# Optimization experiments

Hardware: AMD Instinct MI355X
Metric: run time of the kernel (lower is better)

Reference implementation:

```python
import jax, jax.numpy as jnp
import numpy as np

N_NODES = 50000
N_EDGES = 800000
D = 128
N_LAYERS = 3
EPS = 1e-5


def _layer_norm(x, g, b):
    mu = jnp.mean(x, axis=-1, keepdims=True)
    var = jnp.mean(jnp.square(x - mu), axis=-1, keepdims=True)
    return (x - mu) * jax.lax.rsqrt(var + EPS) * g + b


def _sage_layer(h, src, dst, wl, bl_, wr, g, b):
    # mean aggregation of neighbor (source) features at destination nodes
    msg = h[src]                                             # [E, D] irregular gather
    agg = jax.ops.segment_sum(msg, dst, num_segments=N_NODES)
    deg = jax.ops.segment_sum(jnp.ones((src.shape[0],), h.dtype), dst, num_segments=N_NODES)
    mean = agg / jnp.maximum(deg, 1.0)[:, None]
    # SAGEConv: lin_l(mean_neigh) + lin_r(x); lin_r has no bias
    out = mean @ wl.T + bl_ + h @ wr.T
    h_new = jax.nn.relu(_layer_norm(out, g, b))
    return h + h_new                                          # residual (dims match)


def setup_inputs() -> dict:
    key = jax.random.key(0)
    ks = jax.random.split(key, 5)
    scale = 1.0 / np.sqrt(D)
    node_features = jax.random.normal(ks[0], (N_NODES, D), dtype=jnp.float32)
    edge_index = jax.random.randint(ks[1], (2, N_EDGES), 0, N_NODES, dtype=jnp.int64)
    Wl = jax.random.normal(ks[2], (N_LAYERS, D, D), dtype=jnp.float32) * scale
    Wr = jax.random.normal(ks[3], (N_LAYERS, D, D), dtype=jnp.float32) * scale
    bl = jnp.zeros((N_LAYERS, D), dtype=jnp.float32)
    gamma = jnp.ones((N_LAYERS, D), dtype=jnp.float32)
    beta = jnp.zeros((N_LAYERS, D), dtype=jnp.float32)
    return {"node_features": node_features, "edge_index": edge_index,
            "Wl": Wl, "bl": bl, "Wr": Wr, "gamma": gamma, "beta": beta}


def reference(node_features, edge_index, Wl, bl, Wr, gamma, beta):
    src, dst = edge_index[0], edge_index[1]
    h = node_features
    for i in range(N_LAYERS):
        h = _sage_layer(h, src, dst, Wl[i], bl[i], Wr[i], gamma[i], beta[i])
    return h
```

## Files before the change

### kernel.cpp

```cpp
#include <hip/hip_runtime.h>

#define N_NODES 50000
#define N_EDGES 800000
#define D       128
#define THREADS 256
#define EPS     1e-5f
#define SCAN_B  196
#define MTILES  3125

typedef __attribute__((ext_vector_type(8))) __bf16  bf16x8;
typedef __attribute__((ext_vector_type(8))) short   short8;
typedef __attribute__((ext_vector_type(4))) float   f32x4;
typedef __attribute__((ext_vector_type(4))) unsigned int u32x4;

__device__ inline unsigned int bfround(float x) {
    unsigned int u = __float_as_uint(x);
    return (u + 0x7FFFu + ((u >> 16) & 1u)) >> 16;
}
__device__ inline unsigned int packbf(float x) {
    unsigned int hi = bfround(x);
    float lo = x - __uint_as_float(hi << 16);
    return (hi << 16) | (bfround(lo) & 0xFFFFu);
}
__device__ inline float unpackbf(unsigned int u) {
    return __uint_as_float(u & 0xFFFF0000u) + __uint_as_float(u << 16);
}


__global__ void count_kernel(const int* __restrict__ dst, int* __restrict__ deg) {
    int e = blockIdx.x * 256 + threadIdx.x;
    if (e < N_EDGES) atomicAdd(&deg[dst[e]], 1);
}

__global__ void block_reduce_kernel(const int* __restrict__ deg, int* __restrict__ bsum) {
    __shared__ int red[256];
    int i = blockIdx.x * 256 + threadIdx.x;
    red[threadIdx.x] = (i < N_NODES) ? deg[i] : 0;
    __syncthreads();
    for (int off = 128; off > 0; off >>= 1) {
        if (threadIdx.x < off) red[threadIdx.x] += red[threadIdx.x + off];
        __syncthreads();
    }
    if (threadIdx.x == 0) bsum[blockIdx.x] = red[0];
}

__global__ void block_scan_kernel(const int* __restrict__ bsum, int* __restrict__ bbase) {
    __shared__ int s[256];
    const int t = threadIdx.x;
    const int v = (t < SCAN_B) ? bsum[t] : 0;
    s[t] = v;
    __syncthreads();
    for (int off = 1; off < 256; off <<= 1) {
        int add = (t >= off) ? s[t - off] : 0;
        __syncthreads();
        s[t] += add;
        __syncthreads();
    }
    if (t < SCAN_B) bbase[t] = s[t] - v;
}

__global__ void expand_kernel(const int* __restrict__ deg, const int* __restrict__ bbase,
                              int* __restrict__ row_start, int* __restrict__ cursor) {
    __shared__ int s[256];
    const int t = threadIdx.x;
    const int i = blockIdx.x * 256 + t;
    const int v = (i < N_NODES) ? deg[i] : 0;
    s[t] = v;
    __syncthreads();
    for (int off = 1; off < 256; off <<= 1) {
        int add = (t >= off) ? s[t - off] : 0;
        __syncthreads();
        s[t] += add;
        __syncthreads();
    }
    const int excl = bbase[blockIdx.x] + s[t] - v;
    if (i < N_NODES) { row_start[i] = excl; cursor[i] = excl; }
    if (i == N_NODES - 1) row_start[N_NODES] = excl + v;
}

__global__ void fill_kernel(const int* __restrict__ src, const int* __restrict__ dst,
                            int* __restrict__ cursor, int* __restrict__ ssrc) {
    int e = blockIdx.x * 256 + threadIdx.x;
    if (e < N_EDGES) {
        int d = dst[e];
        int p = atomicAdd(&cursor[d], 1);
        __builtin_nontemporal_store(src[e], &ssrc[p]);
    }
}


__global__ void wprep_kernel(const float* __restrict__ Wl, const float* __restrict__ Wr,
                             unsigned short* __restrict__ Whi, unsigned short* __restrict__ Wlo) {
    int t = blockIdx.x * 256 + threadIdx.x;
    if (t >= 3 * 128 * 256) return;
    const int L = t >> 15;
    const int r = t & 32767;
    const int j = r >> 8;
    const int k = r & 255;
    const float x = (k < 128) ? Wl[((size_t)L * 128 + j) * 128 + k]
                              : Wr[((size_t)L * 128 + j) * 128 + (k - 128)];
    const unsigned int p = packbf(x);
    Whi[t] = (unsigned short)(p >> 16);
    Wlo[t] = (unsigned short)(p & 0xFFFFu);
}

__global__ void cvt0_kernel(const float* __restrict__ nf,
                            unsigned int* __restrict__ Apk,
                            unsigned short* __restrict__ Hh) {
    int t = blockIdx.x * 256 + threadIdx.x;
    if (t >= N_NODES * 32) return;
    const int n  = t >> 5;
    const int k4 = (t & 31) * 4;
    const float4 v = *reinterpret_cast<const float4*>(nf + (size_t)n * D + k4);
    u32x4 o;
    o.x = packbf(v.x); o.y = packbf(v.y); o.z = packbf(v.z); o.w = packbf(v.w);
    *reinterpret_cast<u32x4*>(Apk + (size_t)n * 128 + k4) = o;
    uint2 hh;
    hh.x = (o.x >> 16) | (o.y & 0xFFFF0000u);
    hh.y = (o.z >> 16) | (o.w & 0xFFFF0000u);
    *reinterpret_cast<uint2*>((unsigned int*)Hh + (size_t)n * 64 + (k4 >> 1)) = hh;
}


__global__ __launch_bounds__(256, 8)
void agg_kernel(const unsigned short* __restrict__ Hh,
                unsigned short* __restrict__ Mb,
                const int* __restrict__ row_start, const int* __restrict__ ssrc) {
    const int lane = threadIdx.x & 63;
    const int wave = threadIdx.x >> 6;
    const int n = blockIdx.x * 4 + wave;
    if (n >= N_NODES) return;
    const int e0 = __builtin_amdgcn_readfirstlane(row_start[n]);
    const int e1 = __builtin_amdgcn_readfirstlane(row_start[n + 1]);
    const unsigned int* __restrict__ H = (const unsigned int*)Hh + lane;

    float a0 = 0.f, a1 = 0.f;
    #pragma unroll 1
    for (int e = e0; e < e1; e += 16) {
        const int el = e1 - 1;
        const int s0  = ssrc[min(e + 0,  el)];
        const int s1  = ssrc[min(e + 1,  el)];
        const int s2  = ssrc[min(e + 2,  el)];
        const int s3  = ssrc[min(e + 3,  el)];
        const int s4  = ssrc[min(e + 4,  el)];
        const int s5  = ssrc[min(e + 5,  el)];
        const int s6  = ssrc[min(e + 6,  el)];
        const int s7  = ssrc[min(e + 7,  el)];
        const int s8  = ssrc[min(e + 8,  el)];
        const int s9  = ssrc[min(e + 9,  el)];
        const int s10 = ssrc[min(e + 10, el)];
        const int s11 = ssrc[min(e + 11, el)];
        const int s12 = ssrc[min(e + 12, el)];
        const int s13 = ssrc[min(e + 13, el)];
        const int s14 = ssrc[min(e + 14, el)];
        const int s15 = ssrc[min(e + 15, el)];
        const unsigned int v0  = H[(size_t)s0  * 64];
        const unsigned int v1  = H[(size_t)s1  * 64];
        const unsigned int v2  = H[(size_t)s2  * 64];
        const unsigned int v3  = H[(size_t)s3  * 64];
        const unsigned int v4  = H[(size_t)s4  * 64];
        const unsigned int v5  = H[(size_t)s5  * 64];
        const unsigned int v6  = H[(size_t)s6  * 64];
        const unsigned int v7  = H[(size_t)s7  * 64];
        const unsigned int v8  = H[(size_t)s8  * 64];
        const unsigned int v9  = H[(size_t)s9  * 64];
        const unsigned int v10 = H[(size_t)s10 * 64];
        const unsigned int v11 = H[(size_t)s11 * 64];
        const unsigned int v12 = H[(size_t)s12 * 64];
        const unsigned int v13 = H[(size_t)s13 * 64];
        const unsigned int v14 = H[(size_t)s14 * 64];
        const unsigned int v15 = H[(size_t)s15 * 64];
        const float w1  = (e + 1  < e1) ? 1.f : 0.f;
        const float w2  = (e + 2  < e1) ? 1.f : 0.f;
        const float w3  = (e + 3  < e1) ? 1.f : 0.f;
        const float w4  = (e + 4  < e1) ? 1.f : 0.f;
        const float w5  = (e + 5  < e1) ? 1.f : 0.f;
        const float w6  = (e + 6  < e1) ? 1.f : 0.f;
        const float w7  = (e + 7  < e1) ? 1.f : 0.f;
        const float w8  = (e + 8  < e1) ? 1.f : 0.f;
        const float w9  = (e + 9  < e1) ? 1.f : 0.f;
        const float w10 = (e + 10 < e1) ? 1.f : 0.f;
        const float w11 = (e + 11 < e1) ? 1.f : 0.f;
        const float w12 = (e + 12 < e1) ? 1.f : 0.f;
        const float w13 = (e + 13 < e1) ? 1.f : 0.f;
        const float w14 = (e + 14 < e1) ? 1.f : 0.f;
        const float w15 = (e + 15 < e1) ? 1.f : 0.f;
        a0 += __uint_as_float(v0 << 16);
        a1 += __uint_as_float(v0 & 0xFFFF0000u);
        a0 = fmaf(__uint_as_float(v1  << 16), w1,  a0);  a1 = fmaf(__uint_as_float(v1  & 0xFFFF0000u), w1,  a1);
        a0 = fmaf(__uint_as_float(v2  << 16), w2,  a0);  a1 = fmaf(__uint_as_float(v2  & 0xFFFF0000u), w2,  a1);
        a0 = fmaf(__uint_as_float(v3  << 16), w3,  a0);  a1 = fmaf(__uint_as_float(v3  & 0xFFFF0000u), w3,  a1);
        a0 = fmaf(__uint_as_float(v4  << 16), w4,  a0);  a1 = fmaf(__uint_as_float(v4  & 0xFFFF0000u), w4,  a1);
        a0 = fmaf(__uint_as_float(v5  << 16), w5,  a0);  a1 = fmaf(__uint_as_float(v5  & 0xFFFF0000u), w5,  a1);
        a0 = fmaf(__uint_as_float(v6  << 16), w6,  a0);  a1 = fmaf(__uint_as_float(v6  & 0xFFFF0000u), w6,  a1);
        a0 = fmaf(__uint_as_float(v7  << 16), w7,  a0);  a1 = fmaf(__uint_as_float(v7  & 0xFFFF0000u), w7,  a1);
        a0 = fmaf(__uint_as_float(v8  << 16), w8,  a0);  a1 = fmaf(__uint_as_float(v8  & 0xFFFF0000u), w8,  a1);
        a0 = fmaf(__uint_as_float(v9  << 16), w9,  a0);  a1 = fmaf(__uint_as_float(v9  & 0xFFFF0000u), w9,  a1);
        a0 = fmaf(__uint_as_float(v10 << 16), w10, a0);  a1 = fmaf(__uint_as_float(v10 & 0xFFFF0000u), w10, a1);
        a0 = fmaf(__uint_as_float(v11 << 16), w11, a0);  a1 = fmaf(__uint_as_float(v11 & 0xFFFF0000u), w11, a1);
        a0 = fmaf(__uint_as_float(v12 << 16), w12, a0);  a1 = fmaf(__uint_as_float(v12 & 0xFFFF0000u), w12, a1);
        a0 = fmaf(__uint_as_float(v13 << 16), w13, a0);  a1 = fmaf(__uint_as_float(v13 & 0xFFFF0000u), w13, a1);
        a0 = fmaf(__uint_as_float(v14 << 16), w14, a0);  a1 = fmaf(__uint_as_float(v14 & 0xFFFF0000u), w14, a1);
        a0 = fmaf(__uint_as_float(v15 << 16), w15, a0);  a1 = fmaf(__uint_as_float(v15 & 0xFFFF0000u), w15, a1);
    }
    const float inv = 1.f / (float)max(e1 - e0, 1);
    const unsigned int w = bfround(a0 * inv) | (bfround(a1 * inv) << 16);
    ((unsigned int*)Mb)[(size_t)n * 64 + lane] = w;
}


template<int MODE>
__global__ __launch_bounds__(256, 4)
void gemm_kernel(unsigned int* __restrict__ Apk,
                 unsigned short* __restrict__ Hh,
                 const unsigned short* __restrict__ Mb,
                 float* __restrict__ outF,
                 const unsigned short* __restrict__ Whi,
                 const unsigned short* __restrict__ Wlo,
                 const float* __restrict__ bl,
                 const float* __restrict__ gamma,
                 const float* __restrict__ beta) {
    __shared__ unsigned short Bs[2][16][64][8];

    const int tid  = threadIdx.x;
    const int lane = tid & 63;
    const int wave = tid >> 6;
    const int mt0  = blockIdx.x * 4 + wave;
    const int mt   = min(mt0, MTILES - 1);
    const int rl   = lane & 15;
    const int kg   = lane >> 4;
    const int n    = mt * 16 + rl;
    const int slot = rl * 4 + kg;

    bf16x8 AM[4];
    {
        const unsigned int* __restrict__ mr =
            (const unsigned int*)Mb + (size_t)n * 64 + kg * 4;
        #pragma unroll
        for (int kt = 0; kt < 4; ++kt) {
            u32x4 m = *reinterpret_cast<const u32x4*>(mr + kt * 16);
            asm volatile("" : "+v"(m));
            AM[kt] = __builtin_bit_cast(bf16x8, m);
        }
    }
    bf16x8 AH[4], AL[4];
    {
        const unsigned int* __restrict__ ar = Apk + (size_t)n * 128 + kg * 8;
        #pragma unroll
        for (int kt = 0; kt < 4; ++kt) {
            const u32x4 p = *reinterpret_cast<const u32x4*>(ar + kt * 32);
            const u32x4 q = *reinterpret_cast<const u32x4*>(ar + kt * 32 + 4);
            u32x4 hw, lw;
            hw.x = (p.y & 0xFFFF0000u) | (p.x >> 16);
            hw.y = (p.w & 0xFFFF0000u) | (p.z >> 16);
            hw.z = (q.y & 0xFFFF0000u) | (q.x >> 16);
            hw.w = (q.w & 0xFFFF0000u) | (q.z >> 16);
            lw.x = (p.x & 0xFFFFu) | (p.y << 16);
            lw.y = (p.z & 0xFFFFu) | (p.w << 16);
            lw.z = (q.x & 0xFFFFu) | (q.y << 16);
            lw.w = (q.z & 0xFFFFu) | (q.w << 16);
            asm volatile("" : "+v"(hw), "+v"(lw));
            AH[kt] = __builtin_bit_cast(bf16x8, hw);
            AL[kt] = __builtin_bit_cast(bf16x8, lw);
        }
    }

    f32x4 AC[8];
    #pragma unroll
    for (int jt = 0; jt < 8; ++jt) { AC[jt].x = 0.f; AC[jt].y = 0.f; AC[jt].z = 0.f; AC[jt].w = 0.f; }

    #pragma unroll
    for (int qu = 0; qu < 4; ++qu) {
        if (qu) __syncthreads();

        #pragma unroll
        for (int q = 0; q < 4; ++q) {
            const int c  = q * 256 + tid;
            const int j  = c >> 3;
            const int G  = c & 7;
            const size_t gsrc = (size_t)j * 256 + qu * 64 + G * 8;
            const short8 vh = *reinterpret_cast<const short8*>(Whi + gsrc);
            const short8 vl = *reinterpret_cast<const short8*>(Wlo + gsrc);
            const int tile = (j >> 4) * 2 + (G >> 2);
            const int slw  = (j & 15) * 4 + (G & 3);
            *reinterpret_cast<short8*>(&Bs[0][tile][slw][0]) = vh;
            *reinterpret_cast<short8*>(&Bs[1][tile][slw][0]) = vl;
        }
        __syncthreads();

        #pragma unroll
        for (int jt = 0; jt < 8; ++jt) {
            #pragma unroll
            for (int ktl = 0; ktl < 2; ++ktl) {
                const bf16x8 BH = __builtin_bit_cast(bf16x8,
                    *reinterpret_cast<const short8*>(&Bs[0][jt * 2 + ktl][slot][0]));
                const bf16x8 BL = __builtin_bit_cast(bf16x8,
                    *reinterpret_cast<const short8*>(&Bs[1][jt * 2 + ktl][slot][0]));
                const int ka = qu * 2 + ktl;
                if (ka < 4) {
                    AC[jt] = __builtin_amdgcn_mfma_f32_16x16x32_bf16(AM[ka], BH, AC[jt], 0, 0, 0);
                    AC[jt] = __builtin_amdgcn_mfma_f32_16x16x32_bf16(AM[ka], BL, AC[jt], 0, 0, 0);
                } else {
                    AC[jt] = __builtin_amdgcn_mfma_f32_16x16x32_bf16(AH[ka - 4], BH, AC[jt], 0, 0, 0);
                    AC[jt] = __builtin_amdgcn_mfma_f32_16x16x32_bf16(AL[ka - 4], BH, AC[jt], 0, 0, 0);
                    AC[jt] = __builtin_amdgcn_mfma_f32_16x16x32_bf16(AH[ka - 4], BL, AC[jt], 0, 0, 0);
                }
            }
        }
    }

    #pragma unroll
    for (int jt = 0; jt < 8; ++jt) {
        const float bb = bl[jt * 16 + rl];
        AC[jt].x += bb; AC[jt].y += bb; AC[jt].z += bb; AC[jt].w += bb;
    }

    float mu[4], rs[4];
    #pragma unroll
    for (int r = 0; r < 4; ++r) {
        float s1 = 0.f, s2 = 0.f;
        #pragma unroll
        for (int jt = 0; jt < 8; ++jt) {
            const float v = AC[jt][r];
            s1 += v;
            s2 = fmaf(v, v, s2);
        }
        #pragma unroll
        for (int m = 1; m < 16; m <<= 1) {
            s1 += __shfl_xor(s1, m);
            s2 += __shfl_xor(s2, m);
        }
        mu[r] = s1 * (1.f / 128.f);
        const float var = fmaf(s2, 1.f / 128.f, -mu[r] * mu[r]);
        rs[r] = 1.f / sqrtf(var + EPS);
    }

    if (mt0 < MTILES) {
        #pragma unroll
        for (int jt = 0; jt < 8; ++jt) {
            const int j = jt * 16 + rl;
            const float g  = gamma[j];
            const float be = beta[j];
            #pragma unroll
            for (int r = 0; r < 4; ++r) {
                const int row = mt * 16 + kg * 4 + r;
                unsigned int* hp = Apk + (size_t)row * 128 + j;
                const float res = unpackbf(*hp);
                const float v = fmaxf(fmaf((AC[jt][r] - mu[r]) * rs[r], g, be), 0.f);
                const float o = res + v;
                if (MODE == 0) {
                    const unsigned int pk = packbf(o);
                    *hp = pk;
                    Hh[(size_t)row * D + j] = (unsigned short)(pk >> 16);
                } else {
                    outF[(size_t)row * D + j] = o;
                }
            }
        }
    }
}


extern "C" void kernel_launch(void* const* d_in, const int* in_sizes, int n_in,
                              void* d_out, int out_size, void* d_ws, size_t ws_size,
                              hipStream_t stream) {
    const float* nf = (const float*)d_in[0];
    const int*   ei = (const int*)d_in[1];
    const float* Wl = (const float*)d_in[2];
    const float* bl = (const float*)d_in[3];
    const float* Wr = (const float*)d_in[4];
    const float* gm = (const float*)d_in[5];
    const float* bt = (const float*)d_in[6];
    float* out = (float*)d_out;

    char* w = (char*)d_ws;
    size_t off = 0;
    auto carve = [&](size_t bytes) -> char* {
        char* p = w + off;
        off = (off + bytes + 511) & ~(size_t)511;
        return p;
    };
    int*   deg       = (int*)carve((size_t)N_NODES * 4);
    int*   row_start = (int*)carve((size_t)(N_NODES + 1) * 4);
    int*   cursor    = (int*)carve((size_t)N_NODES * 4);
    int*   bsum      = (int*)carve((size_t)SCAN_B * 4);
    int*   bbase     = (int*)carve((size_t)SCAN_B * 4);
    int*   ssrc      = (int*)carve((size_t)N_EDGES * 4);
    unsigned int*   Apk = (unsigned int*)carve((size_t)N_NODES * 128 * 4);
    unsigned short* Hh  = (unsigned short*)carve((size_t)N_NODES * 128 * 2);
    unsigned short* Mb  = (unsigned short*)carve((size_t)N_NODES * 128 * 2);
    unsigned short* Whi = (unsigned short*)carve((size_t)3 * 128 * 256 * 2);
    unsigned short* Wlo = (unsigned short*)carve((size_t)3 * 128 * 256 * 2);

    const int* src = ei;
    const int* dst = ei + N_EDGES;

    hipMemsetAsync(deg, 0, (size_t)N_NODES * 4, stream);
    count_kernel<<<(N_EDGES + 255) / 256, 256, 0, stream>>>(dst, deg);
    block_reduce_kernel<<<SCAN_B, 256, 0, stream>>>(deg, bsum);
    block_scan_kernel<<<1, 256, 0, stream>>>(bsum, bbase);
    expand_kernel<<<SCAN_B, 256, 0, stream>>>(deg, bbase, row_start, cursor);
    fill_kernel<<<(N_EDGES + 255) / 256, 256, 0, stream>>>(src, dst, cursor, ssrc);

    wprep_kernel<<<(3 * 128 * 256 + 255) / 256, 256, 0, stream>>>(Wl, Wr, Whi, Wlo);
    cvt0_kernel<<<(N_NODES * 32 + 255) / 256, 256, 0, stream>>>(nf, Apk, Hh);

    const int GA = (N_NODES + 3) / 4;
    const int GG = (MTILES + 3) / 4;

    agg_kernel<<<GA, THREADS, 0, stream>>>(Hh, Mb, row_start, ssrc);
    gemm_kernel<0><<<GG, THREADS, 0, stream>>>(Apk, Hh, Mb, nullptr, Whi, Wlo, bl, gm, bt);
    agg_kernel<<<GA, THREADS, 0, stream>>>(Hh, Mb, row_start, ssrc);
    gemm_kernel<0><<<GG, THREADS, 0, stream>>>(Apk, Hh, Mb, nullptr,
                                               Whi + 32768, Wlo + 32768,
                                               bl + D, gm + D, bt + D);
    agg_kernel<<<GA, THREADS, 0, stream>>>(Hh, Mb, row_start, ssrc);
    gemm_kernel<1><<<GG, THREADS, 0, stream>>>(Apk, Hh, Mb, out,
                                               Whi + 65536, Wlo + 65536,
                                               bl + 2 * D, gm + 2 * D, bt + 2 * D);
}
```

Measured before the change: 365.9 us.

## Build CSR via two-level binned scatter with shared-memory local sort

Replaces the global-atomic degree count, multi-kernel scan and atomic fill with a binned approach. Edges are scattered into 128-node bins using per-block LDS histograms, then each bin is counting-sorted in shared memory to produce row_start and ssrc. This cuts kernel launches and contended global atomics. In exchange it caps each bin at a fixed capacity, which would silently drop edges on skewed degree distributions.

```diff
diff --git a/kernel.cpp b/kernel.cpp
--- a/kernel.cpp
+++ b/kernel.cpp
@@ -5,8 +5,11 @@
 #define D       128
 #define THREADS 256
 #define EPS     1e-5f
-#define SCAN_B  196
 #define MTILES  3125
+#define NBINS   391
+#define BINCAP  4096
+#define SCAT_B  196
+#define EPB     4096
 
 typedef __attribute__((ext_vector_type(8))) __bf16  bf16x8;
 typedef __attribute__((ext_vector_type(8))) short   short8;
@@ -27,64 +30,96 @@
 }
 
 
-__global__ void count_kernel(const int* __restrict__ dst, int* __restrict__ deg) {
-    int e = blockIdx.x * 256 + threadIdx.x;
-    if (e < N_EDGES) atomicAdd(&deg[dst[e]], 1);
-}
-
-__global__ void block_reduce_kernel(const int* __restrict__ deg, int* __restrict__ bsum) {
-    __shared__ int red[256];
-    int i = blockIdx.x * 256 + threadIdx.x;
-    red[threadIdx.x] = (i < N_NODES) ? deg[i] : 0;
-    __syncthreads();
-    for (int off = 128; off > 0; off >>= 1) {
-        if (threadIdx.x < off) red[threadIdx.x] += red[threadIdx.x + off];
+__global__ __launch_bounds__(THREADS)
+void binscatter_kernel(const int* __restrict__ src, const int* __restrict__ dst,
+                       int* __restrict__ bincnt, uint2* __restrict__ binbuf) {
+    __shared__ int hist[NBINS];
+    __shared__ int base[NBINS];
+    const int tid = threadIdx.x;
+    for (int t = tid; t < NBINS; t += THREADS) hist[t] = 0;
+    __syncthreads();
+    const int e0 = blockIdx.x * EPB;
+    #pragma unroll 1
+    for (int r = 0; r < EPB / THREADS; ++r) {
+        const int e = e0 + r * THREADS + tid;
+        if (e < N_EDGES) atomicAdd(&hist[dst[e] >> 7], 1);
+    }
+    __syncthreads();
+    for (int t = tid; t < NBINS; t += THREADS) {
+        const int h = hist[t];
+        base[t] = h ? atomicAdd(&bincnt[t], h) : 0;
+        hist[t] = 0;
+    }
+    __syncthreads();
+    #pragma unroll 1
+    for (int r = 0; r < EPB / THREADS; ++r) {
+        const int e = e0 + r * THREADS + tid;
+        if (e < N_EDGES) {
+            const int d = dst[e];
+            const int b = d >> 7;
+            const int p = base[b] + atomicAdd(&hist[b], 1);
+            if (p < BINCAP)
+                binbuf[(size_t)b * BINCAP + p] = make_uint2((unsigned)src[e], (unsigned)d);
+        }
+    }
+}
+
+__global__ __launch_bounds__(512)
+void binscan_kernel(const int* __restrict__ bincnt, int* __restrict__ binbase,
+                    int* __restrict__ row_start) {
+    __shared__ int s[512];
+    const int t = threadIdx.x;
+    const int v = (t < NBINS) ? bincnt[t] : 0;
+    s[t] = v;
+    __syncthreads();
+    for (int off = 1; off < 512; off <<= 1) {
+        const int a = (t >= off) ? s[t - off] : 0;
         __syncthreads();
-    }
-    if (threadIdx.x == 0) bsum[blockIdx.x] = red[0];
-}
-
-__global__ void block_scan_kernel(const int* __restrict__ bsum, int* __restrict__ bbase) {
-    __shared__ int s[256];
-    const int t = threadIdx.x;
-    const int v = (t < SCAN_B) ? bsum[t] : 0;
-    s[t] = v;
-    __syncthreads();
-    for (int off = 1; off < 256; off <<= 1) {
-        int add = (t >= off) ? s[t - off] : 0;
+        s[t] += a;
         __syncthreads();
-        s[t] += add;
+    }
+    if (t < NBINS) binbase[t] = s[t] - v;
+    if (t == 0) row_start[N_NODES] = N_EDGES;
+}
+
+__global__ __launch_bounds__(THREADS)
+void csrbin_kernel(const int* __restrict__ bincnt, const int* __restrict__ binbase,
+                   const uint2* __restrict__ binbuf,
+                   int* __restrict__ row_start, int* __restrict__ ssrc) {
+    __shared__ uint2 ec[BINCAP];
+    __shared__ int cnt[128], exc[128], cur[128];
+    const int tid = threadIdx.x;
+    const int b   = blockIdx.x;
+    const int nb  = min(bincnt[b], BINCAP);
+    const int gb  = binbase[b];
+    if (tid < 128) { cnt[tid] = 0; cur[tid] = 0; }
+    __syncthreads();
+    #pragma unroll 1
+    for (int i = tid; i < nb; i += THREADS) {
+        const uint2 e = binbuf[(size_t)b * BINCAP + i];
+        ec[i] = e;
+        atomicAdd(&cnt[e.y & 127], 1);
+    }
+    __syncthreads();
+    if (tid < 128) exc[tid] = cnt[tid];
+    __syncthreads();
+    for (int off = 1; off < 128; off <<= 1) {
+        const int a = (tid < 128 && tid >= off) ? exc[tid - off] : 0;
         __syncthreads();
-    }
-    if (t < SCAN_B) bbase[t] = s[t] - v;
-}
-
-__global__ void expand_kernel(const int* __restrict__ deg, const int* __restrict__ bbase,
-                              int* __restrict__ row_start, int* __restrict__ cursor) {
-    __shared__ int s[256];
-    const int t = threadIdx.x;
-    const int i = blockIdx.x * 256 + t;
-    const int v = (i < N_NODES) ? deg[i] : 0;
-    s[t] = v;
-    __syncthreads();
-    for (int off = 1; off < 256; off <<= 1) {
-        int add = (t >= off) ? s[t - off] : 0;
+        if (tid < 128) exc[tid] += a;
         __syncthreads();
-        s[t] += add;
-        __syncthreads();
-    }
-    const int excl = bbase[blockIdx.x] + s[t] - v;
-    if (i < N_NODES) { row_start[i] = excl; cursor[i] = excl; }
-    if (i == N_NODES - 1) row_start[N_NODES] = excl + v;
-}
-
-__global__ void fill_kernel(const int* __restrict__ src, const int* __restrict__ dst,
-                            int* __restrict__ cursor, int* __restrict__ ssrc) {
-    int e = blockIdx.x * 256 + threadIdx.x;
-    if (e < N_EDGES) {
-        int d = dst[e];
-        int p = atomicAdd(&cursor[d], 1);
-        __builtin_nontemporal_store(src[e], &ssrc[p]);
+    }
+    if (tid < 128) {
+        const int n = b * 128 + tid;
+        if (n < N_NODES) row_start[n] = gb + exc[tid] - cnt[tid];
+    }
+    __syncthreads();
+    #pragma unroll 1
+    for (int i = tid; i < nb; i += THREADS) {
+        const uint2 e = ec[i];
+        const int nl = e.y & 127;
+        const int p  = atomicAdd(&cur[nl], 1);
+        ssrc[gb + exc[nl] - cnt[nl] + p] = (int)e.x;
     }
 }
 
@@ -380,12 +415,11 @@
         off = (off + bytes + 511) & ~(size_t)511;
         return p;
     };
-    int*   deg       = (int*)carve((size_t)N_NODES * 4);
+    int*   bincnt    = (int*)carve((size_t)NBINS * 4);
+    int*   binbase   = (int*)carve((size_t)NBINS * 4);
     int*   row_start = (int*)carve((size_t)(N_NODES + 1) * 4);
-    int*   cursor    = (int*)carve((size_t)N_NODES * 4);
-    int*   bsum      = (int*)carve((size_t)SCAN_B * 4);
-    int*   bbase     = (int*)carve((size_t)SCAN_B * 4);
     int*   ssrc      = (int*)carve((size_t)N_EDGES * 4);
+    uint2* binbuf    = (uint2*)carve((size_t)NBINS * BINCAP * 8);
     unsigned int*   Apk = (unsigned int*)carve((size_t)N_NODES * 128 * 4);
     unsigned short* Hh  = (unsigned short*)carve((size_t)N_NODES * 128 * 2);
     unsigned short* Mb  = (unsigned short*)carve((size_t)N_NODES * 128 * 2);
@@ -395,12 +429,10 @@
     const int* src = ei;
     const int* dst = ei + N_EDGES;
 
-    hipMemsetAsync(deg, 0, (size_t)N_NODES * 4, stream);
-    count_kernel<<<(N_EDGES + 255) / 256, 256, 0, stream>>>(dst, deg);
-    block_reduce_kernel<<<SCAN_B, 256, 0, stream>>>(deg, bsum);
-    block_scan_kernel<<<1, 256, 0, stream>>>(bsum, bbase);
-    expand_kernel<<<SCAN_B, 256, 0, stream>>>(deg, bbase, row_start, cursor);
-    fill_kernel<<<(N_EDGES + 255) / 256, 256, 0, stream>>>(src, dst, cursor, ssrc);
+    hipMemsetAsync(bincnt, 0, (size_t)NBINS * 4, stream);
+    binscatter_kernel<<<SCAT_B, THREADS, 0, stream>>>(src, dst, bincnt, binbuf);
+    binscan_kernel<<<1, 512, 0, stream>>>(bincnt, binbase, row_start);
+    csrbin_kernel<<<NBINS, THREADS, 0, stream>>>(bincnt, binbase, binbuf, row_start, ssrc);
 
     wprep_kernel<<<(3 * 128 * 256 + 255) / 256, 256, 0, stream>>>(Wl, Wr, Whi, Wlo);
     cvt0_kernel<<<(N_NODES * 32 + 255) / 256, 256, 0, stream>>>(nf, Apk, Hh);
```

Result: faster. 300.1 us (-18.0%).
